# Kernel optimization log

Hardware: AMD Instinct MI355X
Metric: run time of the kernel (lower is better)

## Reference

```python
import jax, jax.numpy as jnp
import numpy as np

B, S, H = 4, 512, 1024
E, K, I = 8, 2, 2048

def setup_inputs() -> dict:
    key = jax.random.key(0)
    k1, k2, k3, k4, k5 = jax.random.split(key, 5)
    scale_h = 1.0 / np.sqrt(H)
    scale_i = 1.0 / np.sqrt(I)
    return {
        "hidden_states": jax.random.normal(k1, (B, S, H), dtype=jnp.float32),
        "router_w": jax.random.normal(k2, (E, H), dtype=jnp.float32) * scale_h,
        "w_gate": jax.random.normal(k3, (E, H, I), dtype=jnp.float32) * scale_h,
        "w_up": jax.random.normal(k4, (E, H, I), dtype=jnp.float32) * scale_h,
        "w_down": jax.random.normal(k5, (E, I, H), dtype=jnp.float32) * scale_i,
    }

def reference(hidden_states, router_w, w_gate, w_up, w_down):
    b, s, h = hidden_states.shape
    x = hidden_states.reshape(-1, h)              # [T, H] tokens
    T = x.shape[0]

    # ---- RouterTopK: fp32 linear -> softmax over all experts -> top-k ----
    router_logits = x.astype(jnp.float32) @ router_w.T          # [T, E]
    probs = jax.nn.softmax(router_logits, axis=-1)               # [T, E]
    top_vals, top_idx = jax.lax.top_k(probs, K)                  # [T, K]

    # normalize_top_k_affinities (norm_topk_prob=True)
    top_vals = top_vals / jnp.sum(top_vals, axis=-1, keepdims=True)

    # scatter normalized affinities into a dense [T, E] combine matrix
    aff = jnp.zeros((T, E), dtype=x.dtype).at[jnp.arange(T)[:, None], top_idx].set(top_vals.astype(x.dtype))

    # ---- ExpertMLPs: GLU (swiglu) per expert, combine weighted by affinity ----
    # Dense-per-expert computation; non-selected experts contribute 0 via aff.
    gate = jnp.einsum('th,ehi->eti', x, w_gate)                  # [E, T, I]
    up = jnp.einsum('th,ehi->eti', x, w_up)                      # [E, T, I]
    act = jax.nn.silu(gate) * up                                 # [E, T, I]
    expert_out = jnp.einsum('eti,eih->eth', act, w_down)         # [E, T, H]
    out = jnp.einsum('eth,te->th', expert_out, aff)              # [T, H]

    # _reduce_output: all-reduce over TP/world group -> identity single-device
    return out.reshape(b, s, h)
```

## Files before the change

kernel.cpp:

```cpp
#include <hip/hip_runtime.h>
#include <hip/hip_bf16.h>

#define T_TOK 2048
#define H_DIM 1024
#define E_N   8
#define I_DIM 2048
#define GW    4096

#define NT_MAX 40
#define SLOTS  5120

typedef unsigned short u16;
typedef unsigned int   u32;
typedef __bf16 bf16_t;
typedef bf16_t bf16x8 __attribute__((ext_vector_type(8)));
typedef u16    u16x8  __attribute__((ext_vector_type(8)));
typedef u16    u16x4  __attribute__((ext_vector_type(4)));
typedef float  f32x16 __attribute__((ext_vector_type(16)));

#define MFMA32 __builtin_amdgcn_mfma_f32_32x32x16_bf16

__device__ __forceinline__ u16 bfbits(float f) {
    bf16_t b = (bf16_t)f;
    return __builtin_bit_cast(u16, b);
}
__device__ __forceinline__ float bf2f(u16 u) {
    u32 x = ((u32)u) << 16;
    return __builtin_bit_cast(float, x);
}

__device__ __forceinline__ void gload_lds16(const void* g, void* l) {
    __builtin_amdgcn_global_load_lds(
        (const __attribute__((address_space(1))) void*)g,
        (__attribute__((address_space(3))) void*)l, 16, 0, 0);
}

__device__ __forceinline__ int tile_off(int n, int kb) {
    return n * 64 + ((kb ^ ((n >> 1) & 7)) << 3);
}
__device__ __forceinline__ int a_off(int row, int kslot) {
    return row * 64 + ((kslot ^ (row & 7)) << 3);
}

__global__ __launch_bounds__(256) void router_k(
    const float* __restrict__ x, const float* __restrict__ rw,
    int* __restrict__ cnt, int* __restrict__ tok,
    int4* __restrict__ invA, float2* __restrict__ invW,
    u16* __restrict__ xbf)
{
    int wid = threadIdx.x >> 6, lane = threadIdx.x & 63;
    int t = blockIdx.x * 4 + wid;
    const float* xr = x + (size_t)t * H_DIM;
    u16* xbr = xbf + (size_t)t * H_DIM;

    float acc[E_N];
#pragma unroll
    for (int e = 0; e < E_N; e++) acc[e] = 0.f;
    for (int j = 0; j < H_DIM / 64; j++) {
        float xv = xr[lane + 64 * j];
        xbr[lane + 64 * j] = bfbits(xv);
#pragma unroll
        for (int e = 0; e < E_N; e++)
            acc[e] += xv * rw[e * H_DIM + lane + 64 * j];
    }
#pragma unroll
    for (int e = 0; e < E_N; e++) {
        float v = acc[e];
        for (int off = 32; off; off >>= 1) v += __shfl_xor(v, off);
        acc[e] = v;
    }
    if (lane == 0) {
        int i0 = 0; float m0 = acc[0];
#pragma unroll
        for (int e = 1; e < E_N; e++) if (acc[e] > m0) { m0 = acc[e]; i0 = e; }
        int i1 = -1; float m1 = -INFINITY;
#pragma unroll
        for (int e = 0; e < E_N; e++) if (e != i0 && acc[e] > m1) { m1 = acc[e]; i1 = e; }
        float w0 = 1.f / (1.f + expf(m1 - m0));
        float w1 = 1.f - w0;
        int p0 = atomicAdd(&cnt[i0], 1);
        tok[i0 * T_TOK + p0] = t;
        int p1 = atomicAdd(&cnt[i1], 1);
        tok[i1 * T_TOK + p1] = t;
        invA[t] = make_int4(i0, p0, i1, p1);
        invW[t] = make_float2(w0, w1);
    }
}

__global__ void prefix_k(const int* __restrict__ cnt, int* __restrict__ offs_pad,
                         int* __restrict__ tile_e, int* __restrict__ tile_row0,
                         int* __restrict__ ntiles)
{
    if (threadIdx.x == 0) {
        int s = 0, nt = 0;
        for (int e = 0; e < E_N; e++) {
            offs_pad[e] = s;
            int c = cnt[e];
            int t = (c + 127) >> 7;
            for (int i = 0; i < t; i++) { tile_e[nt] = e; tile_row0[nt] = i * 128; nt++; }
            s += t * 128;
        }
        offs_pad[E_N] = s;
        *ntiles = nt;
    }
}

__global__ __launch_bounds__(256, 3) void gu_k(
    const u16* __restrict__ xbf, const float* __restrict__ wg, const float* __restrict__ wu,
    const int* __restrict__ cnt, const int* __restrict__ offs_pad,
    const int* __restrict__ tile_e, const int* __restrict__ tile_row0,
    const int* __restrict__ ntiles, const int* __restrict__ tok,
    u16* __restrict__ gbuf)
{
    int q = gridDim.x >> 3;
    int phys = blockIdx.x;
    int logical = (phys & 7) * q + (phys >> 3);
    int tb = logical % NT_MAX;
    int p  = logical / NT_MAX;
    if (tb >= *ntiles) return;
    int e = tile_e[tb], row0 = tile_row0[tb];
    int cntE = cnt[e];
    int slot0 = offs_pad[e] + row0;
    int n0 = p * 128;
    int mat  = n0 >> 11;
    int coln = n0 & 2047;

    __shared__ u16 AS[8192], BS[8192];

    int tid = threadIdx.x;
    int lane = tid & 63, wid = tid >> 6;
    int wm = wid >> 1, wn = wid & 1;
    int l31 = lane & 31, lh = lane >> 5;

    const u16* asrc[4];
#pragma unroll
    for (int i = 0; i < 4; i++) {
        int row = (wid * 4 + i) * 8 + (lane >> 3);
        int rc = (row0 + row < cntE) ? (row0 + row) : (cntE - 1);
        asrc[i] = xbf + (size_t)tok[e * T_TOK + rc] * H_DIM
                  + (((lane & 7) ^ ((lane >> 3) & 7)) << 3);
    }
    int s0 = wid * 2048;

    int bn = tid & 127;
    int khalf = tid >> 7;
    const float* wsrc = (mat ? wu : wg) + (size_t)e * H_DIM * I_DIM + coln + bn;

    float v[32];

#define BLOAD(t) { \
    _Pragma("unroll") \
    for (int j = 0; j < 32; j++) \
        v[j] = wsrc[(size_t)((t) * 64 + khalf * 32 + j) * I_DIM]; }

#define BWRITE() { \
    _Pragma("unroll") \
    for (int jb = 0; jb < 4; jb++) { \
        u16x8 pk; \
        _Pragma("unroll") \
        for (int jj = 0; jj < 8; jj++) pk[jj] = bfbits(v[jb * 8 + jj]); \
        *reinterpret_cast<u16x8*>(&BS[tile_off(bn, khalf * 4 + jb)]) = pk; } }

#define ASTAGE(t) { \
    _Pragma("unroll") \
    for (int i = 0; i < 4; i++) \
        gload_lds16(asrc[i] + (size_t)(t) * 64, &AS[s0 + i * 512]); }

    f32x16 acc[2][2];
#pragma unroll
    for (int a = 0; a < 2; a++)
#pragma unroll
        for (int b = 0; b < 2; b++) acc[a][b] = (f32x16)0.f;

    BLOAD(0);
    for (int t = 0; t < 16; t++) {
        ASTAGE(t);
        BWRITE();
        __syncthreads();
        if (t + 1 < 16) BLOAD(t + 1);
#pragma unroll
        for (int ks = 0; ks < 4; ks++) {
            bf16x8 af[2], bfr[2];
#pragma unroll
            for (int mf = 0; mf < 2; mf++)
                af[mf] = *reinterpret_cast<const bf16x8*>(&AS[a_off(wm * 64 + mf * 32 + l31, ks * 2 + lh)]);
#pragma unroll
            for (int nf = 0; nf < 2; nf++)
                bfr[nf] = *reinterpret_cast<const bf16x8*>(&BS[tile_off(wn * 64 + nf * 32 + l31, ks * 2 + lh)]);
#pragma unroll
            for (int mf = 0; mf < 2; mf++)
#pragma unroll
                for (int nf = 0; nf < 2; nf++)
                    acc[mf][nf] = MFMA32(af[mf], bfr[nf], acc[mf][nf], 0, 0, 0);
        }
        asm volatile("s_waitcnt lgkmcnt(0)" ::: "memory");
        __builtin_amdgcn_s_barrier();
        __builtin_amdgcn_sched_barrier(0);
    }
#undef BLOAD
#undef BWRITE
#undef ASTAGE

#pragma unroll
    for (int mf = 0; mf < 2; mf++)
#pragma unroll
        for (int nf = 0; nf < 2; nf++) {
            int col = n0 + wn * 64 + nf * 32 + l31;
#pragma unroll
            for (int r = 0; r < 16; r++) {
                int rl = wm * 64 + mf * 32 + (r & 3) + 8 * (r >> 2) + 4 * lh;
                gbuf[(size_t)(slot0 + rl) * GW + col] = bfbits(acc[mf][nf][r]);
            }
        }
}

__global__ __launch_bounds__(256) void act_k(const u16* __restrict__ gbuf,
                                             u16* __restrict__ act)
{
    int s = blockIdx.x;
    int i = threadIdx.x * 8;
    u16x8 g8 = *reinterpret_cast<const u16x8*>(&gbuf[(size_t)s * GW + i]);
    u16x8 u8 = *reinterpret_cast<const u16x8*>(&gbuf[(size_t)s * GW + 2048 + i]);
    u16x8 o;
#pragma unroll
    for (int j = 0; j < 8; j++) {
        float g = bf2f(g8[j]);
        float u = bf2f(u8[j]);
        o[j] = bfbits(g / (1.f + expf(-g)) * u);
    }
    *reinterpret_cast<u16x8*>(&act[(size_t)s * I_DIM + i]) = o;
}

__global__ __launch_bounds__(256, 3) void down_k(
    const u16* __restrict__ act, const float* __restrict__ wd,
    const int* __restrict__ cnt, const int* __restrict__ offs_pad,
    const int* __restrict__ tile_e, const int* __restrict__ tile_row0,
    const int* __restrict__ ntiles, const int* __restrict__ tok,
    u16* __restrict__ dbuf)
{
    int q = gridDim.x >> 3;
    int phys = blockIdx.x;
    int logical = (phys & 7) * q + (phys >> 3);
    int tb = logical % NT_MAX;
    int rest = logical / NT_MAX;
    int p  = rest & 7;
    int kh = rest >> 3;
    if (tb >= *ntiles) return;
    int e = tile_e[tb], row0 = tile_row0[tb];
    int slot0 = offs_pad[e] + row0;
    int h0 = p * 128;

    __shared__ u16 AS[8192], BS[8192];

    int tid = threadIdx.x;
    int lane = tid & 63, wid = tid >> 6;
    int wm = wid >> 1, wn = wid & 1;
    int l31 = lane & 31, lh = lane >> 5;

    const u16* asrc[4];
#pragma unroll
    for (int i = 0; i < 4; i++) {
        int row = (wid * 4 + i) * 8 + (lane >> 3);
        asrc[i] = act + (size_t)(slot0 + row) * I_DIM + kh * 1024
                  + (((lane & 7) ^ ((lane >> 3) & 7)) << 3);
    }
    int s0 = wid * 2048;

    int bn = tid & 127;
    int khalf = tid >> 7;
    const float* dsrc = wd + ((size_t)e * I_DIM + kh * 1024) * H_DIM + h0 + bn;

    float v[32];

#define BLOAD(t) { \
    _Pragma("unroll") \
    for (int j = 0; j < 32; j++) \
        v[j] = dsrc[(size_t)((t) * 64 + khalf * 32 + j) * H_DIM]; }

#define BWRITE() { \
    _Pragma("unroll") \
    for (int jb = 0; jb < 4; jb++) { \
        u16x8 pk; \
        _Pragma("unroll") \
        for (int jj = 0; jj < 8; jj++) pk[jj] = bfbits(v[jb * 8 + jj]); \
        *reinterpret_cast<u16x8*>(&BS[tile_off(bn, khalf * 4 + jb)]) = pk; } }

#define ASTAGE(t) { \
    _Pragma("unroll") \
    for (int i = 0; i < 4; i++) \
        gload_lds16(asrc[i] + (size_t)(t) * 64, &AS[s0 + i * 512]); }

    f32x16 acc[2][2];
#pragma unroll
    for (int a = 0; a < 2; a++)
#pragma unroll
        for (int b = 0; b < 2; b++) acc[a][b] = (f32x16)0.f;

    BLOAD(0);
    for (int t = 0; t < 16; t++) {
        ASTAGE(t);
        BWRITE();
        __syncthreads();
        if (t + 1 < 16) BLOAD(t + 1);
#pragma unroll
        for (int ks = 0; ks < 4; ks++) {
            bf16x8 af[2], bfr[2];
#pragma unroll
            for (int mf = 0; mf < 2; mf++)
                af[mf] = *reinterpret_cast<const bf16x8*>(&AS[a_off(wm * 64 + mf * 32 + l31, ks * 2 + lh)]);
#pragma unroll
            for (int nf = 0; nf < 2; nf++)
                bfr[nf] = *reinterpret_cast<const bf16x8*>(&BS[tile_off(wn * 64 + nf * 32 + l31, ks * 2 + lh)]);
#pragma unroll
            for (int mf = 0; mf < 2; mf++)
#pragma unroll
                for (int nf = 0; nf < 2; nf++)
                    acc[mf][nf] = MFMA32(af[mf], bfr[nf], acc[mf][nf], 0, 0, 0);
        }
        asm volatile("s_waitcnt lgkmcnt(0)" ::: "memory");
        __builtin_amdgcn_s_barrier();
        __builtin_amdgcn_sched_barrier(0);
    }
#undef BLOAD
#undef BWRITE
#undef ASTAGE

#pragma unroll
    for (int mf = 0; mf < 2; mf++)
#pragma unroll
        for (int nf = 0; nf < 2; nf++) {
            int col = h0 + wn * 64 + nf * 32 + l31;
#pragma unroll
            for (int r = 0; r < 16; r++) {
                int rl = wm * 64 + mf * 32 + (r & 3) + 8 * (r >> 2) + 4 * lh;
                dbuf[(size_t)(kh * SLOTS + slot0 + rl) * H_DIM + col] = bfbits(acc[mf][nf][r]);
            }
        }
}

__global__ __launch_bounds__(256) void gather_k(
    const u16* __restrict__ dbuf, const int4* __restrict__ invA,
    const float2* __restrict__ invW, const int* __restrict__ offs_pad,
    float* __restrict__ out)
{
    int t = blockIdx.x;
    int h = threadIdx.x * 4;
    int4 ia = invA[t];
    float2 w = invW[t];
    int s0 = offs_pad[ia.x] + ia.y;
    int s1 = offs_pad[ia.z] + ia.w;

    u16x4 a0 = *reinterpret_cast<const u16x4*>(&dbuf[(size_t)s0 * H_DIM + h]);
    u16x4 a1 = *reinterpret_cast<const u16x4*>(&dbuf[(size_t)(SLOTS + s0) * H_DIM + h]);
    u16x4 b0 = *reinterpret_cast<const u16x4*>(&dbuf[(size_t)s1 * H_DIM + h]);
    u16x4 b1 = *reinterpret_cast<const u16x4*>(&dbuf[(size_t)(SLOTS + s1) * H_DIM + h]);

    float4 o;
    float* op = &o.x;
#pragma unroll
    for (int j = 0; j < 4; j++)
        op[j] = w.x * (bf2f(a0[j]) + bf2f(a1[j])) + w.y * (bf2f(b0[j]) + bf2f(b1[j]));
    *reinterpret_cast<float4*>(&out[(size_t)t * H_DIM + h]) = o;
}

extern "C" void kernel_launch(void* const* d_in, const int* in_sizes, int n_in,
                              void* d_out, int out_size, void* d_ws, size_t ws_size,
                              hipStream_t stream)
{
    const float* x  = (const float*)d_in[0];
    const float* rw = (const float*)d_in[1];
    const float* wg = (const float*)d_in[2];
    const float* wu = (const float*)d_in[3];
    const float* wd = (const float*)d_in[4];
    float* out = (float*)d_out;

    char* ws = (char*)d_ws;
    int*    cnt       = (int*)(ws);
    int*    ntiles    = (int*)(ws + 32);
    int*    offs_pad  = (int*)(ws + 64);
    int*    tile_e    = (int*)(ws + 256);
    int*    tile_row0 = (int*)(ws + 512);
    int*    tok       = (int*)(ws + 64 * 1024);
    int4*   invA      = (int4*)(ws + 160 * 1024);
    float2* invW      = (float2*)(ws + 200 * 1024);
    u16*    xbf       = (u16*)(ws + 256 * 1024);
    u16*    act       = (u16*)(ws + 5ull * 1024 * 1024);
    u16*    gbuf      = (u16*)(ws + 26ull * 1024 * 1024);
    u16*    dbuf      = (u16*)(ws + 67ull * 1024 * 1024);

    size_t need = 88ull * 1024 * 1024;
    if (ws_size < need) return;

    hipMemsetAsync(cnt, 0, 32, stream);

    router_k<<<T_TOK / 4, 256, 0, stream>>>(x, rw, cnt, tok, invA, invW, xbf);
    prefix_k<<<1, 64, 0, stream>>>(cnt, offs_pad, tile_e, tile_row0, ntiles);
    gu_k<<<NT_MAX * (GW / 128), 256, 0, stream>>>(
        xbf, wg, wu, cnt, offs_pad, tile_e, tile_row0, ntiles, tok, gbuf);
    act_k<<<SLOTS, 256, 0, stream>>>(gbuf, act);
    down_k<<<NT_MAX * (H_DIM / 128) * 2, 256, 0, stream>>>(
        act, wd, cnt, offs_pad, tile_e, tile_row0, ntiles, tok, dbuf);
    gather_k<<<T_TOK, 256, 0, stream>>>(dbuf, invA, invW, offs_pad, out);
}
```

Before: 205.8 us.

## Pre-convert gate/up weights to swizzled bf16 tiles and double-buffer B via LDS DMA

A new prep kernel, fused with the router, converts the fp32 gate and up weights once per call into pre-swizzled bf16 tiles. The gate/up GEMM can then stream B tiles straight into double-buffered LDS with global_load_lds, and it reads A fragments directly from global memory instead of staging them in LDS. This removes the strided fp32 column loads and per-iteration conversion from the GEMM main loop, at the cost of an extra pass that reads the weights and writes a bf16 copy. The router loads are vectorised to float4, the activation is written in place into gbuf, and the workspace is compacted so dbuf aliases the weight-tile buffer.

```diff
diff --git a/kernel.cpp b/kernel.cpp
--- a/kernel.cpp
+++ b/kernel.cpp
@@ -19,6 +19,7 @@
 typedef float  f32x16 __attribute__((ext_vector_type(16)));
 
 #define MFMA32 __builtin_amdgcn_mfma_f32_32x32x16_bf16
+#define SB()   __builtin_amdgcn_sched_barrier(0)
 
 __device__ __forceinline__ u16 bfbits(float f) {
     bf16_t b = (bf16_t)f;
@@ -42,26 +43,65 @@
     return row * 64 + ((kslot ^ (row & 7)) << 3);
 }
 
-__global__ __launch_bounds__(256) void router_k(
+__global__ __launch_bounds__(256) void prep_k(
     const float* __restrict__ x, const float* __restrict__ rw,
+    const float* __restrict__ wg, const float* __restrict__ wu,
+    u16* __restrict__ tgu,
     int* __restrict__ cnt, int* __restrict__ tok,
     int4* __restrict__ invA, float2* __restrict__ invW,
     u16* __restrict__ xbf)
 {
+    int bid = blockIdx.x;
+    if (bid < 4096) {
+        __shared__ float S[64][132];
+        int kind = bid >> 11;
+        int ti = bid & 2047;
+        int e = ti >> 8, np = (ti >> 4) & 15, kb = ti & 15;
+        const float* w = kind ? wu : wg;
+        const float* src = w + ((size_t)e * H_DIM + kb * 64) * I_DIM + np * 128;
+        u16* dst = tgu + (((size_t)e * 32 + kind * 16 + np) * 16 + kb) * 8192;
+        int tid = threadIdx.x;
+#pragma unroll
+        for (int i = 0; i < 8; i++) {
+            int idx = tid + i * 256;
+            int k = idx >> 5, c4 = idx & 31;
+            float4 v = *reinterpret_cast<const float4*>(src + (size_t)k * I_DIM + c4 * 4);
+            *reinterpret_cast<float4*>(&S[k][c4 * 4]) = v;
+        }
+        __syncthreads();
+#pragma unroll
+        for (int i = 0; i < 4; i++) {
+            int c = tid + i * 256;
+            int n = c >> 3, kbx = c & 7;
+            int k0 = (kbx ^ ((n >> 1) & 7)) << 3;
+            u16x8 pk;
+#pragma unroll
+            for (int j = 0; j < 8; j++) pk[j] = bfbits(S[k0 + j][n]);
+            *reinterpret_cast<u16x8*>(dst + (size_t)c * 8) = pk;
+        }
+        return;
+    }
+
     int wid = threadIdx.x >> 6, lane = threadIdx.x & 63;
-    int t = blockIdx.x * 4 + wid;
+    int t = (bid - 4096) * 4 + wid;
     const float* xr = x + (size_t)t * H_DIM;
     u16* xbr = xbf + (size_t)t * H_DIM;
 
     float acc[E_N];
 #pragma unroll
     for (int e = 0; e < E_N; e++) acc[e] = 0.f;
-    for (int j = 0; j < H_DIM / 64; j++) {
-        float xv = xr[lane + 64 * j];
-        xbr[lane + 64 * j] = bfbits(xv);
-#pragma unroll
-        for (int e = 0; e < E_N; e++)
-            acc[e] += xv * rw[e * H_DIM + lane + 64 * j];
+#pragma unroll
+    for (int j = 0; j < H_DIM / 256; j++) {
+        int o = lane * 4 + j * 256;
+        float4 xv = *reinterpret_cast<const float4*>(xr + o);
+        u16x4 p;
+        p[0] = bfbits(xv.x); p[1] = bfbits(xv.y); p[2] = bfbits(xv.z); p[3] = bfbits(xv.w);
+        *reinterpret_cast<u16x4*>(xbr + o) = p;
+#pragma unroll
+        for (int e = 0; e < E_N; e++) {
+            float4 wv = *reinterpret_cast<const float4*>(rw + e * H_DIM + o);
+            acc[e] += xv.x * wv.x + xv.y * wv.y + xv.z * wv.z + xv.w * wv.w;
+        }
     }
 #pragma unroll
     for (int e = 0; e < E_N; e++) {
@@ -106,7 +146,7 @@
 }
 
 __global__ __launch_bounds__(256, 3) void gu_k(
-    const u16* __restrict__ xbf, const float* __restrict__ wg, const float* __restrict__ wu,
+    const u16* __restrict__ xbf, const u16* __restrict__ tgu,
     const int* __restrict__ cnt, const int* __restrict__ offs_pad,
     const int* __restrict__ tile_e, const int* __restrict__ tile_row0,
     const int* __restrict__ ntiles, const int* __restrict__ tok,
@@ -122,49 +162,29 @@
     int cntE = cnt[e];
     int slot0 = offs_pad[e] + row0;
     int n0 = p * 128;
-    int mat  = n0 >> 11;
-    int coln = n0 & 2047;
-
-    __shared__ u16 AS[8192], BS[8192];
+
+    __shared__ u16 BT[2][8192];
 
     int tid = threadIdx.x;
     int lane = tid & 63, wid = tid >> 6;
     int wm = wid >> 1, wn = wid & 1;
     int l31 = lane & 31, lh = lane >> 5;
 
-    const u16* asrc[4];
-#pragma unroll
-    for (int i = 0; i < 4; i++) {
-        int row = (wid * 4 + i) * 8 + (lane >> 3);
+    const u16* arowp[2];
+#pragma unroll
+    for (int mf = 0; mf < 2; mf++) {
+        int row = wm * 64 + mf * 32 + l31;
         int rc = (row0 + row < cntE) ? (row0 + row) : (cntE - 1);
-        asrc[i] = xbf + (size_t)tok[e * T_TOK + rc] * H_DIM
-                  + (((lane & 7) ^ ((lane >> 3) & 7)) << 3);
-    }
-    int s0 = wid * 2048;
-
-    int bn = tid & 127;
-    int khalf = tid >> 7;
-    const float* wsrc = (mat ? wu : wg) + (size_t)e * H_DIM * I_DIM + coln + bn;
-
-    float v[32];
-
-#define BLOAD(t) { \
-    _Pragma("unroll") \
-    for (int j = 0; j < 32; j++) \
-        v[j] = wsrc[(size_t)((t) * 64 + khalf * 32 + j) * I_DIM]; }
-
-#define BWRITE() { \
-    _Pragma("unroll") \
-    for (int jb = 0; jb < 4; jb++) { \
-        u16x8 pk; \
-        _Pragma("unroll") \
-        for (int jj = 0; jj < 8; jj++) pk[jj] = bfbits(v[jb * 8 + jj]); \
-        *reinterpret_cast<u16x8*>(&BS[tile_off(bn, khalf * 4 + jb)]) = pk; } }
-
-#define ASTAGE(t) { \
-    _Pragma("unroll") \
-    for (int i = 0; i < 4; i++) \
-        gload_lds16(asrc[i] + (size_t)(t) * 64, &AS[s0 + i * 512]); }
+        arowp[mf] = xbf + (size_t)tok[e * T_TOK + rc] * H_DIM;
+    }
+
+    const u16* tbase = tgu + (((size_t)e * 32 + p) * 16) * 8192;
+
+#define BSTAGE(bufi, t) {                                                        \
+    _Pragma("unroll")                                                            \
+    for (int i = 0; i < 4; i++)                                                  \
+        gload_lds16(tbase + (size_t)(t) * 8192 + ((size_t)(wid * 256 + i * 64 + lane)) * 8, \
+                    &BT[bufi][(wid * 256 + i * 64) * 8]); }
 
     f32x16 acc[2][2];
 #pragma unroll
@@ -172,34 +192,32 @@
 #pragma unroll
         for (int b = 0; b < 2; b++) acc[a][b] = (f32x16)0.f;
 
-    BLOAD(0);
+#define CLUSTER(bufi, k0) {                                                      \
+    _Pragma("unroll")                                                            \
+    for (int ksl = 0; ksl < 4; ksl++) {                                          \
+        bf16x8 af[2], bfr[2];                                                    \
+        _Pragma("unroll")                                                        \
+        for (int mf = 0; mf < 2; mf++)                                           \
+            af[mf] = *reinterpret_cast<const bf16x8*>(arowp[mf] + (k0) + ksl * 16 + lh * 8); \
+        _Pragma("unroll")                                                        \
+        for (int nf = 0; nf < 2; nf++)                                           \
+            bfr[nf] = *reinterpret_cast<const bf16x8*>(&BT[bufi][tile_off(wn * 64 + nf * 32 + l31, ksl * 2 + lh)]); \
+        _Pragma("unroll")                                                        \
+        for (int mf = 0; mf < 2; mf++)                                           \
+            _Pragma("unroll")                                                    \
+            for (int nf = 0; nf < 2; nf++)                                       \
+                acc[mf][nf] = MFMA32(af[mf], bfr[nf], acc[mf][nf], 0, 0, 0); } }
+
+    BSTAGE(0, 0);
+    __syncthreads();
     for (int t = 0; t < 16; t++) {
-        ASTAGE(t);
-        BWRITE();
+        int buf = t & 1;
+        if (t + 1 < 16) BSTAGE(buf ^ 1, t + 1);
+        CLUSTER(buf, t * 64);
         __syncthreads();
-        if (t + 1 < 16) BLOAD(t + 1);
-#pragma unroll
-        for (int ks = 0; ks < 4; ks++) {
-            bf16x8 af[2], bfr[2];
-#pragma unroll
-            for (int mf = 0; mf < 2; mf++)
-                af[mf] = *reinterpret_cast<const bf16x8*>(&AS[a_off(wm * 64 + mf * 32 + l31, ks * 2 + lh)]);
-#pragma unroll
-            for (int nf = 0; nf < 2; nf++)
-                bfr[nf] = *reinterpret_cast<const bf16x8*>(&BS[tile_off(wn * 64 + nf * 32 + l31, ks * 2 + lh)]);
-#pragma unroll
-            for (int mf = 0; mf < 2; mf++)
-#pragma unroll
-                for (int nf = 0; nf < 2; nf++)
-                    acc[mf][nf] = MFMA32(af[mf], bfr[nf], acc[mf][nf], 0, 0, 0);
-        }
-        asm volatile("s_waitcnt lgkmcnt(0)" ::: "memory");
-        __builtin_amdgcn_s_barrier();
-        __builtin_amdgcn_sched_barrier(0);
-    }
-#undef BLOAD
-#undef BWRITE
-#undef ASTAGE
+    }
+#undef BSTAGE
+#undef CLUSTER
 
 #pragma unroll
     for (int mf = 0; mf < 2; mf++)
@@ -214,8 +232,7 @@
         }
 }
 
-__global__ __launch_bounds__(256) void act_k(const u16* __restrict__ gbuf,
-                                             u16* __restrict__ act)
+__global__ __launch_bounds__(256) void act_k(u16* __restrict__ gbuf)
 {
     int s = blockIdx.x;
     int i = threadIdx.x * 8;
@@ -228,11 +245,11 @@
         float u = bf2f(u8[j]);
         o[j] = bfbits(g / (1.f + expf(-g)) * u);
     }
-    *reinterpret_cast<u16x8*>(&act[(size_t)s * I_DIM + i]) = o;
+    *reinterpret_cast<u16x8*>(&gbuf[(size_t)s * GW + i]) = o;
 }
 
 __global__ __launch_bounds__(256, 3) void down_k(
-    const u16* __restrict__ act, const float* __restrict__ wd,
+    const u16* __restrict__ gbuf, const float* __restrict__ wd,
     const int* __restrict__ cnt, const int* __restrict__ offs_pad,
     const int* __restrict__ tile_e, const int* __restrict__ tile_row0,
     const int* __restrict__ ntiles, const int* __restrict__ tok,
@@ -260,8 +277,8 @@
     const u16* asrc[4];
 #pragma unroll
     for (int i = 0; i < 4; i++) {
-        int row = (wid * 4 + i) * 8 + (lane >> 3);
-        asrc[i] = act + (size_t)(slot0 + row) * I_DIM + kh * 1024
+        int row = wid * 32 + i * 8 + (lane >> 3);
+        asrc[i] = gbuf + (size_t)(slot0 + row) * GW + kh * 1024
                   + (((lane & 7) ^ ((lane >> 3) & 7)) << 3);
     }
     int s0 = wid * 2048;
@@ -319,7 +336,7 @@
         }
         asm volatile("s_waitcnt lgkmcnt(0)" ::: "memory");
         __builtin_amdgcn_s_barrier();
-        __builtin_amdgcn_sched_barrier(0);
+        SB();
     }
 #undef BLOAD
 #undef BWRITE
@@ -384,21 +401,22 @@
     int4*   invA      = (int4*)(ws + 160 * 1024);
     float2* invW      = (float2*)(ws + 200 * 1024);
     u16*    xbf       = (u16*)(ws + 256 * 1024);
-    u16*    act       = (u16*)(ws + 5ull * 1024 * 1024);
-    u16*    gbuf      = (u16*)(ws + 26ull * 1024 * 1024);
-    u16*    dbuf      = (u16*)(ws + 67ull * 1024 * 1024);
-
-    size_t need = 88ull * 1024 * 1024;
+    u16*    gbuf      = (u16*)(ws + 4608ull * 1024);
+    u16*    tgu       = (u16*)(ws + 45568ull * 1024);
+    u16*    dbuf      = tgu;
+
+    size_t need = 45568ull * 1024 + 64ull * 1024 * 1024;
     if (ws_size < need) return;
 
     hipMemsetAsync(cnt, 0, 32, stream);
 
-    router_k<<<T_TOK / 4, 256, 0, stream>>>(x, rw, cnt, tok, invA, invW, xbf);
+    prep_k<<<4096 + T_TOK / 4, 256, 0, stream>>>(x, rw, wg, wu, tgu,
+                                                 cnt, tok, invA, invW, xbf);
     prefix_k<<<1, 64, 0, stream>>>(cnt, offs_pad, tile_e, tile_row0, ntiles);
     gu_k<<<NT_MAX * (GW / 128), 256, 0, stream>>>(
-        xbf, wg, wu, cnt, offs_pad, tile_e, tile_row0, ntiles, tok, gbuf);
-    act_k<<<SLOTS, 256, 0, stream>>>(gbuf, act);
+        xbf, tgu, cnt, offs_pad, tile_e, tile_row0, ntiles, tok, gbuf);
+    act_k<<<SLOTS, 256, 0, stream>>>(gbuf);
     down_k<<<NT_MAX * (H_DIM / 128) * 2, 256, 0, stream>>>(
-        act, wd, cnt, offs_pad, tile_e, tile_row0, ntiles, tok, dbuf);
+        gbuf, wd, cnt, offs_pad, tile_e, tile_row0, ntiles, tok, dbuf);
     gather_k<<<T_TOK, 256, 0, stream>>>(dbuf, invA, invW, offs_pad, out);
 }
```

Measured after the change: 260.2 us. +26.4%, slower.
